# Kernel tuning notes

Measured on AMD Instinct MI355X. Metric: run time of the kernel, lower is better.

The kernel has to match this reference:

```python
import jax, jax.numpy as jnp
import numpy as np

# ---- module constants (from init_kwargs) ----
NATOMS = 600
NBINS = 64
CUTOFF = 7.5            # raw cutoff passed to __init__
CELL_L = 20.0           # cubic box edge (diagonal cell)
PI = float(np.pi)

BINS = jnp.linspace(0.0, CUTOFF, NBINS + 1)                 # [nbins+1]
VOL_BINS = 4.0 * PI / 3.0 * (BINS[1:] ** 3 - BINS[:-1] ** 3)  # [nbins]
CUTOFF_ADJ = CUTOFF + float(BINS[1] - BINS[0]) * 2.0        # self.cutoff after init
CELL = jnp.array([CELL_L, CELL_L, CELL_L], dtype=jnp.float32)  # diag of cell

# GaussianSmearing(start=0, stop=cutoff, n_gaussians=nbins, trainable=False)
G_OFFSETS = jnp.linspace(0.0, CUTOFF, NBINS)                # [nbins]
G_WIDTH = float(G_OFFSETS[1] - G_OFFSETS[0])
G_COEFF = -0.5 / (G_WIDTH ** 2)


def setup_inputs() -> dict:
    key = jax.random.key(0)
    # positions uniformly inside the cubic box [0, L)^3
    xyz = jax.random.uniform(key, (4, NATOMS, 3), dtype=jnp.float32) * CELL_L
    return {"xyz": xyz}


def reference(xyz):
    # pairwise differences: [B, N, N, 3]
    dis_mat = xyz[:, None, :, :] - xyz[:, :, None, :]
    # minimum-image PBC wrap
    offsets = (-(dis_mat >= 0.5 * CELL).astype(xyz.dtype)
               + (dis_mat < -0.5 * CELL).astype(xyz.dtype))
    dis_mat = dis_mat + offsets * CELL
    dis_sq = jnp.sum(dis_mat * dis_mat, axis=-1)            # [B, N, N]
    mask = (dis_sq < CUTOFF_ADJ ** 2) & (dis_sq != 0.0)     # [B, N, N]
    # safe sqrt (masked-out entries contribute zero below)
    pair_dis = jnp.sqrt(jnp.where(mask, dis_sq, 1.0))       # [B, N, N]
    # Gaussian smear -> soft histogram: sum over all valid pairs
    gauss = jnp.exp(G_COEFF * (pair_dis[..., None] - G_OFFSETS) ** 2)  # [B,N,N,nbins]
    count = jnp.sum(mask[..., None].astype(xyz.dtype) * gauss, axis=(0, 1, 2))  # [nbins]
    count = count / jnp.sum(count)
    rdf_val = count / (2.0 * VOL_BINS / (2.0 * CUTOFF_ADJ) ** 3)
    return (BINS, rdf_val)
```

## Files before the change

### kernel.cpp

```cpp
#include <hip/hip_runtime.h>
#include <math.h>

#define NATOMS 600
#define NBINS  64
#define NBATCH 4
#define NROWS  (NBATCH * NATOMS)
#define NREPL  32
#define RPB    150

constexpr float CELL_L     = 20.0f;
constexpr float INV_CELL   = 1.0f / 20.0f;
constexpr float BIN_W      = 7.5f / 64.0f;
constexpr float CUTOFF_ADJ = 7.5f + 2.0f * BIN_W;
constexpr float CUT2       = CUTOFF_ADJ * CUTOFF_ADJ;
constexpr float G_SPACING  = 7.5f / 63.0f;
constexpr float G_COEFF    = -0.5f / (G_SPACING * G_SPACING);
constexpr float PI_F       = 3.14159265358979323846f;

__global__ __launch_bounds__(256) void rdf_pairs(const float* __restrict__ xyz,
                                                 float* __restrict__ repl) {
    __shared__ float sflat[NATOMS * 3];
    __shared__ float shits[4][NATOMS + 8];

    const int tid  = threadIdx.x;
    const int wave = tid >> 6;
    const int lane = tid & 63;
    const int bid  = blockIdx.x;
    const int b    = bid / RPB;
    const int g    = bid - b * RPB;
    const int i    = g * 4 + wave;

    const float* gp = xyz + (size_t)b * NATOMS * 3;
    for (int t = tid; t < NATOMS * 3; t += 256) sflat[t] = gp[t];
    __syncthreads();

    const float xi = sflat[3 * i + 0];
    const float yi = sflat[3 * i + 1];
    const float zi = sflat[3 * i + 2];

    int nh = 0;
    for (int j0 = 0; j0 < NATOMS; j0 += 64) {
        const int j = j0 + lane;
        const bool valid = j < NATOMS;
        const int jj = valid ? j : 0;
        float dx = sflat[3 * jj + 0] - xi;
        float dy = sflat[3 * jj + 1] - yi;
        float dz = sflat[3 * jj + 2] - zi;
        dx -= CELL_L * rintf(dx * INV_CELL);
        dy -= CELL_L * rintf(dy * INV_CELL);
        dz -= CELL_L * rintf(dz * INV_CELL);
        const float r2 = dx * dx + dy * dy + dz * dz;
        const float d  = sqrtf(r2);
        const bool hit = valid && (r2 < CUT2) && (r2 != 0.0f);
        const unsigned long long m = __ballot(hit);
        const int prefix = __builtin_amdgcn_mbcnt_hi(
            (unsigned)(m >> 32), __builtin_amdgcn_mbcnt_lo((unsigned)m, 0));
        if (hit) shits[wave][nh + prefix] = d;
        nh += (int)__popcll(m);
    }

    const float off = (float)lane * G_SPACING;
    float acc = 0.0f;
    #pragma unroll 4
    for (int h = 0; h < nh; ++h) {
        const float t = shits[wave][h] - off;
        acc += __expf(G_COEFF * t * t);
    }

    const int gw = (bid << 2) | wave;
    atomicAdd(&repl[(gw & (NREPL - 1)) * NBINS + lane], acc);
}

__global__ __launch_bounds__(64) void rdf_finalize(const float* __restrict__ repl,
                                                   float* __restrict__ out) {
    const int lane = threadIdx.x;
    const float poison = __uint_as_float(0xAAAAAAAAu);
    float c = -(float)NREPL * poison;
    #pragma unroll
    for (int r = 0; r < NREPL; ++r) c += repl[r * NBINS + lane];

    float total = c;
    #pragma unroll
    for (int o = 32; o > 0; o >>= 1) total += __shfl_xor(total, o, 64);

    out[lane] = (float)lane * BIN_W;
    if (lane == 0) out[64] = 7.5f;

    const float b0 = (float)lane * BIN_W;
    const float b1 = (float)(lane + 1) * BIN_W;
    const float vol = (4.0f * PI_F / 3.0f) * (b1 * b1 * b1 - b0 * b0 * b0);
    const float diam = 2.0f * CUTOFF_ADJ;
    const float denom = 2.0f * vol / (diam * diam * diam);
    out[65 + lane] = (c / total) / denom;
}

extern "C" void kernel_launch(void* const* d_in, const int* in_sizes, int n_in,
                              void* d_out, int out_size, void* d_ws, size_t ws_size,
                              hipStream_t stream) {
    const float* xyz = (const float*)d_in[0];
    float* out = (float*)d_out;
    float* repl = (float*)d_ws;

    rdf_pairs<<<dim3(NBATCH * RPB), dim3(256), 0, stream>>>(xyz, repl);
    rdf_finalize<<<dim3(1), dim3(64), 0, stream>>>(repl, out);
}
```

Baseline: 65.10 us.

## Exploit pair symmetry to halve work and fuse finalize via ticket counter

Each wave now handles half of an atom-pair row, split so that every unordered pair (i,j) is visited once instead of twice. This halves the distance and Gaussian-smear work. Because the histogram is normalized by its own sum, the factor of two cancels. The separate finalize kernel is removed: every block increments a global ticket, and block 0 spin-waits on it before reducing the replicas. This relies on the workspace holding a known poison value and on all blocks being co-resident, with a guard bound in case they are not.

```diff
diff --git a/kernel.cpp b/kernel.cpp
--- a/kernel.cpp
+++ b/kernel.cpp
@@ -4,9 +4,10 @@
 #define NATOMS 600
 #define NBINS  64
 #define NBATCH 4
-#define NROWS  (NBATCH * NATOMS)
 #define NREPL  32
-#define RPB    150
+#define BPB    150
+#define NBLOCKS (NBATCH * BPB)
+#define HMAX   304
 
 constexpr float CELL_L     = 20.0f;
 constexpr float INV_CELL   = 1.0f / 20.0f;
@@ -16,82 +17,107 @@
 constexpr float G_SPACING  = 7.5f / 63.0f;
 constexpr float G_COEFF    = -0.5f / (G_SPACING * G_SPACING);
 constexpr float PI_F       = 3.14159265358979323846f;
+constexpr unsigned POISON_U = 0xAAAAAAAAu;
+constexpr unsigned TICKET_TARGET = POISON_U + (unsigned)NBLOCKS;
 
 __global__ __launch_bounds__(256) void rdf_pairs(const float* __restrict__ xyz,
-                                                 float* __restrict__ repl) {
+                                                 float* __restrict__ repl,
+                                                 unsigned* __restrict__ ticket,
+                                                 float* __restrict__ out) {
     __shared__ float sflat[NATOMS * 3];
-    __shared__ float shits[4][NATOMS + 8];
+    __shared__ float shits[4][HMAX];
 
     const int tid  = threadIdx.x;
     const int wave = tid >> 6;
     const int lane = tid & 63;
     const int bid  = blockIdx.x;
-    const int b    = bid / RPB;
-    const int g    = bid - b * RPB;
-    const int i    = g * 4 + wave;
+    const int b    = bid / BPB;
+    const int g    = bid - b * BPB;
+    const int ww   = (g << 2) | wave;
+    const int p    = ww >> 1;
+    const int half = ww & 1;
 
     const float* gp = xyz + (size_t)b * NATOMS * 3;
     for (int t = tid; t < NATOMS * 3; t += 256) sflat[t] = gp[t];
     __syncthreads();
 
-    const float xi = sflat[3 * i + 0];
-    const float yi = sflat[3 * i + 1];
-    const float zi = sflat[3 * i + 2];
+    int nh = 0;
+    float* hb = shits[wave];
 
-    int nh = 0;
-    for (int j0 = 0; j0 < NATOMS; j0 += 64) {
-        const int j = j0 + lane;
-        const bool valid = j < NATOMS;
-        const int jj = valid ? j : 0;
-        float dx = sflat[3 * jj + 0] - xi;
-        float dy = sflat[3 * jj + 1] - yi;
-        float dz = sflat[3 * jj + 2] - zi;
-        dx -= CELL_L * rintf(dx * INV_CELL);
-        dy -= CELL_L * rintf(dy * INV_CELL);
-        dz -= CELL_L * rintf(dz * INV_CELL);
-        const float r2 = dx * dx + dy * dy + dz * dz;
-        const float d  = sqrtf(r2);
-        const bool hit = valid && (r2 < CUT2) && (r2 != 0.0f);
-        const unsigned long long m = __ballot(hit);
-        const int prefix = __builtin_amdgcn_mbcnt_hi(
-            (unsigned)(m >> 32), __builtin_amdgcn_mbcnt_lo((unsigned)m, 0));
-        if (hit) shits[wave][nh + prefix] = d;
-        nh += (int)__popcll(m);
+    auto sweep = [&](int row, int jlo, int cnt) {
+        const float xi = sflat[3 * row + 0];
+        const float yi = sflat[3 * row + 1];
+        const float zi = sflat[3 * row + 2];
+        for (int c = 0; c < cnt; c += 64) {
+            const int idx = c + lane;
+            const bool valid = idx < cnt;
+            const int jj = jlo + (valid ? idx : 0);
+            float dx = sflat[3 * jj + 0] - xi;
+            float dy = sflat[3 * jj + 1] - yi;
+            float dz = sflat[3 * jj + 2] - zi;
+            dx -= CELL_L * rintf(dx * INV_CELL);
+            dy -= CELL_L * rintf(dy * INV_CELL);
+            dz -= CELL_L * rintf(dz * INV_CELL);
+            const float r2 = dx * dx + dy * dy + dz * dz;
+            const float d  = sqrtf(r2);
+            const bool hit = valid && (r2 < CUT2) && (r2 != 0.0f);
+            const unsigned long long m = __ballot(hit);
+            const int prefix = __builtin_amdgcn_mbcnt_hi(
+                (unsigned)(m >> 32), __builtin_amdgcn_mbcnt_lo((unsigned)m, 0));
+            if (hit) hb[nh + prefix] = d;
+            nh += (int)__popcll(m);
+        }
+    };
+
+    if (half == 0) {
+        sweep(p, p + 1, 300);
+    } else {
+        sweep(p, p + 301, 299 - p);
+        sweep(599 - p, 600 - p, p);
     }
 
     const float off = (float)lane * G_SPACING;
     float acc = 0.0f;
     #pragma unroll 4
     for (int h = 0; h < nh; ++h) {
-        const float t = shits[wave][h] - off;
+        const float t = hb[h] - off;
         acc += __expf(G_COEFF * t * t);
     }
 
     const int gw = (bid << 2) | wave;
     atomicAdd(&repl[(gw & (NREPL - 1)) * NBINS + lane], acc);
-}
 
-__global__ __launch_bounds__(64) void rdf_finalize(const float* __restrict__ repl,
-                                                   float* __restrict__ out) {
-    const int lane = threadIdx.x;
-    const float poison = __uint_as_float(0xAAAAAAAAu);
-    float c = -(float)NREPL * poison;
-    #pragma unroll
-    for (int r = 0; r < NREPL; ++r) c += repl[r * NBINS + lane];
+    __syncthreads();
+    if (tid == 0) atomicAdd(ticket, 1u);
 
-    float total = c;
-    #pragma unroll
-    for (int o = 32; o > 0; o >>= 1) total += __shfl_xor(total, o, 64);
+    if (bid == 0 && wave == 0) {
+        int guard = 0;
+        while (__hip_atomic_load(ticket, __ATOMIC_RELAXED,
+                                 __HIP_MEMORY_SCOPE_AGENT) != TICKET_TARGET) {
+            if (++guard > (1 << 17)) break;
+            __builtin_amdgcn_s_sleep(2);
+        }
+        const float poison = __uint_as_float(POISON_U);
+        float c = -(float)NREPL * poison;
+        #pragma unroll
+        for (int r = 0; r < NREPL; ++r)
+            c += __hip_atomic_load(&repl[r * NBINS + lane], __ATOMIC_RELAXED,
+                                   __HIP_MEMORY_SCOPE_AGENT);
 
-    out[lane] = (float)lane * BIN_W;
-    if (lane == 0) out[64] = 7.5f;
+        float total = c;
+        #pragma unroll
+        for (int o = 32; o > 0; o >>= 1) total += __shfl_xor(total, o, 64);
 
-    const float b0 = (float)lane * BIN_W;
-    const float b1 = (float)(lane + 1) * BIN_W;
-    const float vol = (4.0f * PI_F / 3.0f) * (b1 * b1 * b1 - b0 * b0 * b0);
-    const float diam = 2.0f * CUTOFF_ADJ;
-    const float denom = 2.0f * vol / (diam * diam * diam);
-    out[65 + lane] = (c / total) / denom;
+        out[lane] = (float)lane * BIN_W;
+        if (lane == 0) out[64] = 7.5f;
+
+        const float b0 = (float)lane * BIN_W;
+        const float b1 = (float)(lane + 1) * BIN_W;
+        const float vol = (4.0f * PI_F / 3.0f) * (b1 * b1 * b1 - b0 * b0 * b0);
+        const float diam = 2.0f * CUTOFF_ADJ;
+        const float denom = 2.0f * vol / (diam * diam * diam);
+        out[65 + lane] = (c / total) / denom;
+    }
 }
 
 extern "C" void kernel_launch(void* const* d_in, const int* in_sizes, int n_in,
@@ -100,7 +126,7 @@
     const float* xyz = (const float*)d_in[0];
     float* out = (float*)d_out;
     float* repl = (float*)d_ws;
+    unsigned* ticket = (unsigned*)d_ws + NREPL * NBINS;
 
-    rdf_pairs<<<dim3(NBATCH * RPB), dim3(256), 0, stream>>>(xyz, repl);
-    rdf_finalize<<<dim3(1), dim3(64), 0, stream>>>(repl, out);
+    rdf_pairs<<<dim3(NBLOCKS), dim3(256), 0, stream>>>(xyz, repl, ticket, out);
 }
```

After: 66.40 us. About the same (+2.0%).
